# Performance work log

Hardware: AMD Instinct MI355X
Metric: run time of the kernel (lower is better)

## Reference

```python
import jax, jax.numpy as jnp
import numpy as np

N = 1_000_000
L_MAX = 8
NUM_REP = 4
N_SCALARS = 64
ROT_IN = L_MAX * 2 * 2          # 32 (num_rep_in = 2)
ROT_OUT = NUM_REP * L_MAX * 2   # 64
ROT_HID = ROT_OUT * 3           # 192
SC_HID = N_SCALARS * 3          # 192


def setup_inputs() -> dict:
    key = jax.random.key(0)
    ks = jax.random.split(key, 12)
    inp = {
        "v": jax.random.normal(ks[0], (N, 2), jnp.float32),
        "force": jax.random.normal(ks[1], (N, 2), jnp.float32),
        "is_moving": jax.random.randint(ks[2], (N,), 0, 2, jnp.int64),
        "rot_theta": jax.random.normal(ks[3], (N, L_MAX, 2, 2), jnp.float32),
        # scalar MLP params (in=4 -> 192 -> 64)
        "Ws1": jax.random.normal(ks[4], (4, SC_HID), jnp.float32) * 0.1,
        "bs1": jnp.zeros((SC_HID,), jnp.float32),
        "Ws2": jax.random.normal(ks[5], (SC_HID, N_SCALARS), jnp.float32) * 0.1,
        "bs2": jnp.zeros((N_SCALARS,), jnp.float32),
        # rot MLP params (in=32 -> 192 -> 64)
        "Wr1": jax.random.normal(ks[6], (ROT_IN, ROT_HID), jnp.float32) * 0.1,
        "br1": jnp.zeros((ROT_HID,), jnp.float32),
        "Wr2": jax.random.normal(ks[7], (ROT_HID, ROT_OUT), jnp.float32) * 0.1,
        "br2": jnp.zeros((ROT_OUT,), jnp.float32),
    }
    return inp


def _mlp(x, W1, b1, W2, b2):
    return jax.nn.relu(x @ W1 + b1) @ W2 + b2


def reference(v, force, is_moving, rot_theta, Ws1, bs1, Ws2, bs2, Wr1, br1, Wr2, br2):
    n = force.shape[0]
    force_norm = jnp.linalg.norm(force, axis=1)          # [N]
    f_hat = force / force_norm[:, None]
    v_norm = jnp.linalg.norm(v, axis=1)
    v_hat = v / v_norm[:, None]
    theta_f = jnp.arctan2(f_hat[:, 1], f_hat[:, 0])[:, None]  # [N,1]
    theta_v = jnp.arctan2(v_hat[:, 1], v_hat[:, 0])[:, None]

    one_hot = jax.nn.one_hot(is_moving, 2, dtype=force.dtype)  # [N,2]

    k = jnp.arange(1, L_MAX + 1, dtype=force.dtype)[None, :]   # [1,L]
    k_f = theta_f * k                                           # [N,L]
    k_v = theta_v * k
    # stack (cos, sin) along new axis then flatten -> [N, 2*L]
    rot_f = jnp.stack((jnp.cos(k_f), jnp.sin(k_f)), axis=2).reshape(n, L_MAX * 2)
    rot_v = jnp.stack((jnp.cos(k_v), jnp.sin(k_v)), axis=2).reshape(n, L_MAX * 2)

    scalar_features = jnp.concatenate(
        [force_norm[:, None], v_norm[:, None], one_hot], axis=1)  # [N,4]
    scalar_out = _mlp(scalar_features, Ws1, bs1, Ws2, bs2)        # [N,64]

    rot_feat = jnp.stack([rot_f, rot_v], axis=1)                  # [N,2,2L]

    # Rot_embedding2 forward
    rot_theta_inv = jnp.swapaxes(rot_theta, 2, 3)                 # [N,L,2,2]
    x = rot_feat.reshape(n, 2, L_MAX, 2)
    x = jnp.einsum('njkm,nkml->njkl', x, rot_theta_inv).reshape(n, ROT_IN)
    x = _mlp(x, Wr1, br1, Wr2, br2)                               # [N,64]
    x = x.reshape(n, NUM_REP, L_MAX, 2)
    rot_out = jnp.einsum('njkm,nkml->njkl', x, rot_theta).reshape(n, NUM_REP, L_MAX * 2)

    return scalar_out, rot_out
```

## Files before the change

kernel.cpp:

```cpp
#include <hip/hip_runtime.h>
#include <math.h>

typedef short bf16x8 __attribute__((ext_vector_type(8)));
typedef float f32x16 __attribute__((ext_vector_type(16)));
typedef float f32x4v __attribute__((ext_vector_type(4)));
typedef unsigned short u16;
typedef unsigned int u32;

__device__ __forceinline__ u16 f2bf(float x) {
    u32 u = __float_as_uint(x);
    u += 0x7FFFu + ((u >> 16) & 1u);
    return (u16)(u >> 16);
}

__device__ __forceinline__ u32 cvt_pk_bf16(float lo, float hi) {
    u32 r;
    asm("v_cvt_pk_bf16_f32 %0, %1, %2" : "=v"(r) : "v"(lo), "v"(hi));
    return r;
}

__device__ __forceinline__ void pl32_swap(u32 &x, u32 &y) {
    asm volatile("v_permlane32_swap_b32 %0, %1" : "+v"(x), "+v"(y));
}

__device__ __forceinline__ bf16x8 frag_from(u32 a, u32 b, u32 c, u32 d) {
    union { u32 u[4]; bf16x8 v; } t;
    t.u[0] = a; t.u[1] = b; t.u[2] = c; t.u[3] = d;
    return t.v;
}

__global__ void prepack_kernel(const float* __restrict__ Ws1, const float* __restrict__ bs1,
                               const float* __restrict__ Ws2, const float* __restrict__ Wr1,
                               const float* __restrict__ br1, const float* __restrict__ Wr2,
                               u16* __restrict__ ws)
{
    int idx = blockIdx.x * blockDim.x + threadIdx.x;
    if (idx >= 36864) return;
    int e = idx & 511, l = e >> 3, j = e & 7, hi = l >> 5, l31 = l & 31;
    float val = 0.0f;
    if (idx < 12288) {
        int blk = idx >> 9;
        if (blk < 18) {
            int nt = blk / 3, kstep = blk % 3;
            int h = nt * 32 + l31;
            int k = kstep * 16 + 8 * hi + j;
            if (k < 32) {
                int t = k & 3, kk = k >> 2;
                int r_old = (t >> 1) * 16 + 2 * kk + (t & 1);
                val = Wr1[r_old * 192 + h];
            } else if (k == 32) val = br1[h];
        } else {
            int h = (blk - 18) * 32 + l31;
            int k = 32 + 8 * hi + j;
            val = (k == 32) ? bs1[h] : ((k >= 33 && k <= 36) ? Ws1[(k - 33) * 192 + h] : 0.0f);
        }
    } else {
        int t = idx - 12288;
        int blk = t >> 9;
        int mlp = blk / 24, rem = blk % 24, ks = rem >> 1, nto = rem & 1;
        int k = 16 * ks + 8 * hi + j;
        int col = nto * 32 + l31;
        val = (mlp == 0 ? Wr2 : Ws2)[k * 64 + col];
    }
    ws[idx] = f2bf(val);
}

__global__ __launch_bounds__(256, 4) void node_embed_mfma(
    const float* __restrict__ v, const float* __restrict__ force,
    const int* __restrict__ is_moving, const float* __restrict__ rot_theta,
    const float* __restrict__ br2, const float* __restrict__ bs2,
    const u16* __restrict__ wpack,
    float* __restrict__ out, int n)
{
    __shared__ alignas(16)  u16   Buf[4][1280];
    __shared__ alignas(128) float Rs[4][1024];

    const int lane = threadIdx.x & 63;
    const int w    = threadIdx.x >> 6;
    const int hi   = lane >> 5;
    const int l31  = lane & 31;
    const int waveBase = blockIdx.x * 128 + w * 32;

    u16*   Xs  = &Buf[w][0];
    float* Os  = reinterpret_cast<float*>(&Buf[w][0]);
    const char* RsB = reinterpret_cast<const char*>(&Rs[w][0]);

    {
        const char* gbase = reinterpret_cast<const char*>(rot_theta);
        const u32 inner = ((u32)(lane & 7) * 16u) ^ ((u32)(lane >> 3) << 4);
        #pragma unroll
        for (int i = 0; i < 4; ++i) {
            int node_i = waveBase + i * 8 + (lane >> 3);
            node_i = min(node_i, n - 1);
            const void* src = gbase + (size_t)node_i * 128 + inner;
            __builtin_amdgcn_global_load_lds(
                (const __attribute__((address_space(1))) u32*)src,
                (__attribute__((address_space(3))) u32*)(&Rs[w][i * 256]),
                16, 0, 0);
        }
    }

    const int node = waveBase + l31;
    const int ldn  = min(node, n - 1);

    const float2 p2 = *reinterpret_cast<const float2*>((hi ? v : force) + (size_t)ldn * 2);
    const float nrm = sqrtf(p2.x * p2.x + p2.y * p2.y);
    const float c = p2.x / nrm, s = p2.y / nrm;
    const int mov = is_moving[ldn];

    asm volatile("s_waitcnt vmcnt(0)" ::: "memory");

    u16* xrow = Xs + l31 * 40;
    {
        float pc = c, ps = s;
        const u32 rowswz = (u32)(l31 & 7) << 4;
        #pragma unroll
        for (int k = 0; k < 8; ++k) {
            const u32 off = ((u32)(l31 * 128 + k * 16)) ^ rowswz;
            const float4 R = *reinterpret_cast<const float4*>(RsB + off);
            const float e0 = fmaf(R.x, pc, R.y * ps);
            const float e1 = fmaf(R.z, pc, R.w * ps);
            *reinterpret_cast<u32*>(xrow + 4 * k + 2 * hi) = cvt_pk_bf16(e0, e1);
            const float npc = pc * c - ps * s;
            ps = fmaf(ps, c, pc * s);
            pc = npc;
        }
    }
    {
        const u16 nb = f2bf(nrm);
        u32 pk1, pk2;
        if (hi == 0) { pk1 = 0x3F80u | ((u32)nb << 16);
                       pk2 = (mov == 1) ? 0x3F80u : 0u; }
        else         { pk1 = (u32)nb | ((mov == 0) ? 0x3F800000u : 0u);
                       pk2 = 0u; }
        *reinterpret_cast<u32*>(xrow + 32 + 2 * hi) = pk1;
        *reinterpret_cast<u32*>(xrow + 36 + 2 * hi) = pk2;
    }

    const bf16x8 xb0 = *reinterpret_cast<const bf16x8*>(&Xs[l31 * 40 + 8 * hi]);
    const bf16x8 xb1 = *reinterpret_cast<const bf16x8*>(&Xs[l31 * 40 + 16 + 8 * hi]);
    const bf16x8 xq4 = *reinterpret_cast<const bf16x8*>(&Xs[l31 * 40 + 32]);

    const u16* A1 = wpack;
    const u16* W2 = wpack + 12288;

    const int rowl = lane >> 4;
    const int qd   = lane & 15;

    const float b2r_a = br2[l31],      b2r_b = br2[32 + l31];
    const float b2s_a = bs2[l31],      b2s_b = bs2[32 + l31];

    #pragma unroll
    for (int mlp = 0; mlp < 2; ++mlp) {
        const float b2a = mlp ? b2s_a : b2r_a;
        const float b2b = mlp ? b2s_b : b2r_b;

        f32x16 acc0, acc1;
        #pragma unroll
        for (int r = 0; r < 16; ++r) { acc0[r] = b2a; acc1[r] = b2b; }

        #pragma unroll
        for (int a = 0; a < 6; ++a) {
            f32x16 d1;
            #pragma unroll
            for (int r = 0; r < 16; ++r) d1[r] = 0.0f;
            if (mlp == 0) {
                d1 = __builtin_amdgcn_mfma_f32_32x32x16_bf16(
                    *reinterpret_cast<const bf16x8*>(&A1[(a*3+0)*512 + lane*8]), xb0, d1, 0, 0, 0);
                d1 = __builtin_amdgcn_mfma_f32_32x32x16_bf16(
                    *reinterpret_cast<const bf16x8*>(&A1[(a*3+1)*512 + lane*8]), xb1, d1, 0, 0, 0);
                d1 = __builtin_amdgcn_mfma_f32_32x32x16_bf16(
                    *reinterpret_cast<const bf16x8*>(&A1[(a*3+2)*512 + lane*8]), xq4, d1, 0, 0, 0);
            } else {
                d1 = __builtin_amdgcn_mfma_f32_32x32x16_bf16(
                    *reinterpret_cast<const bf16x8*>(&A1[(18+a)*512 + lane*8]), xq4, d1, 0, 0, 0);
            }

            u32 q[8];
            #pragma unroll
            for (int m = 0; m < 8; ++m)
                q[m] = cvt_pk_bf16(fmaxf(d1[2*m], 0.0f), fmaxf(d1[2*m+1], 0.0f));

            #pragma unroll
            for (int b = 0; b < 2; ++b) {
                u32 p0 = q[4*b + 0], p2 = q[4*b + 2];
                u32 p1 = q[4*b + 1], p3 = q[4*b + 3];
                pl32_swap(p0, p2);
                pl32_swap(p1, p3);
                const bf16x8 af = frag_from(p0, p1, p2, p3);
                const int ks = 2*a + b;
                acc0 = __builtin_amdgcn_mfma_f32_32x32x16_bf16(
                    af, *reinterpret_cast<const bf16x8*>(&W2[(mlp*24 + ks*2 + 0)*512 + lane*8]),
                    acc0, 0, 0, 0);
                acc1 = __builtin_amdgcn_mfma_f32_32x32x16_bf16(
                    af, *reinterpret_cast<const bf16x8*>(&W2[(mlp*24 + ks*2 + 1)*512 + lane*8]),
                    acc1, 0, 0, 0);
            }
        }

        #pragma unroll
        for (int rq = 0; rq < 4; ++rq) {
            #pragma unroll
            for (int rr = 0; rr < 4; ++rr) {
                const int r = rq * 4 + rr;
                Os[(rr + 4*hi) * 72 + l31]      = acc0[r];
                Os[(rr + 4*hi) * 72 + 32 + l31] = acc1[r];
            }
            #pragma unroll
            for (int g = 0; g < 2; ++g) {
                const int row   = g * 4 + rowl;
                const int srow  = rq * 8 + row;
                const int node0 = waveBase + srow;
                float4 o = *reinterpret_cast<const float4*>(&Os[row * 72 + 4 * qd]);
                if (mlp == 0) {
                    const u32 roff = ((u32)(srow * 128 + (qd & 3) * 32))
                                   ^ ((u32)(srow & 7) << 4);
                    const float4 Ra = *reinterpret_cast<const float4*>(RsB + roff);
                    const float4 Rc = *reinterpret_cast<const float4*>(RsB + (roff ^ 16u));
                    {
                        const float a0 = o.x, b0 = o.y;
                        o.x = fmaf(a0, Ra.x, b0 * Ra.z); o.y = fmaf(a0, Ra.y, b0 * Ra.w);
                    }
                    {
                        const float a0 = o.z, b0 = o.w;
                        o.z = fmaf(a0, Rc.x, b0 * Rc.z); o.w = fmaf(a0, Rc.y, b0 * Rc.w);
                    }
                }
                if (node0 < n) {
                    float* dst = out + (mlp ? (size_t)0 : (size_t)n * 64)
                                     + (size_t)node0 * 64 + 4 * qd;
                    f32x4v ov;
                    ov[0] = o.x; ov[1] = o.y; ov[2] = o.z; ov[3] = o.w;
                    __builtin_nontemporal_store(ov, reinterpret_cast<f32x4v*>(dst));
                }
            }
        }
    }
}

__global__ __launch_bounds__(256) void node_embed_valu(
    const float* __restrict__ v, const float* __restrict__ force,
    const int* __restrict__ is_moving, const float* __restrict__ rot_theta,
    const float* __restrict__ Ws1, const float* __restrict__ bs1,
    const float* __restrict__ Ws2, const float* __restrict__ bs2,
    const float* __restrict__ Wr1, const float* __restrict__ br1,
    const float* __restrict__ Wr2, const float* __restrict__ br2,
    float* __restrict__ out, int n)
{
    const int node = blockIdx.x * blockDim.x + threadIdx.x;
    if (node >= n) return;
    const float2 f2 = *reinterpret_cast<const float2*>(force + (size_t)node * 2);
    const float2 v2 = *reinterpret_cast<const float2*>(v     + (size_t)node * 2);
    const float fn = sqrtf(f2.x * f2.x + f2.y * f2.y);
    const float vn = sqrtf(v2.x * v2.x + v2.y * v2.y);
    const float cf = f2.x / fn, sf = f2.y / fn;
    const float cv = v2.x / vn, sv = v2.y / vn;
    const int mov = is_moving[node];
    float rotf[16], rotv[16];
    rotf[0] = cf; rotf[1] = sf; rotv[0] = cv; rotv[1] = sv;
    #pragma unroll
    for (int k = 1; k < 8; ++k) {
        rotf[2*k]   = rotf[2*k-2] * cf - rotf[2*k-1] * sf;
        rotf[2*k+1] = rotf[2*k-1] * cf + rotf[2*k-2] * sf;
        rotv[2*k]   = rotv[2*k-2] * cv - rotv[2*k-1] * sv;
        rotv[2*k+1] = rotv[2*k-1] * cv + rotv[2*k-2] * sv;
    }
    const float* Rb = rot_theta + (size_t)node * 32;
    float x_in[32];
    #pragma unroll
    for (int k = 0; k < 8; ++k) {
        const float4 R = *reinterpret_cast<const float4*>(Rb + k * 4);
        { const float a = rotf[2*k], b = rotf[2*k+1];
          x_in[2*k] = fmaf(R.x,a,R.y*b); x_in[2*k+1] = fmaf(R.z,a,R.w*b); }
        { const float a = rotv[2*k], b = rotv[2*k+1];
          x_in[16+2*k] = fmaf(R.x,a,R.y*b); x_in[16+2*k+1] = fmaf(R.z,a,R.w*b); }
    }
    float acc[64];
    #pragma unroll
    for (int j = 0; j < 64; ++j) acc[j] = br2[j];
    for (int h = 0; h < 192; h += 4) {
        float hid[4];
        #pragma unroll
        for (int u = 0; u < 4; ++u) {
            float t = br1[h+u];
            #pragma unroll
            for (int i = 0; i < 32; ++i) t = fmaf(x_in[i], Wr1[i*192+h+u], t);
            hid[u] = fmaxf(t, 0.0f);
        }
        #pragma unroll
        for (int j = 0; j < 64; ++j) {
            float t = acc[j];
            #pragma unroll
            for (int u = 0; u < 4; ++u) t = fmaf(hid[u], Wr2[(h+u)*64+j], t);
            acc[j] = t;
        }
    }
    #pragma unroll
    for (int k = 0; k < 8; ++k) {
        const float4 R = *reinterpret_cast<const float4*>(Rb + k * 4);
        #pragma unroll
        for (int j = 0; j < 4; ++j) {
            const int p = j*16 + 2*k;
            const float a = acc[p], b = acc[p+1];
            acc[p] = fmaf(a,R.x,b*R.z); acc[p+1] = fmaf(a,R.y,b*R.w);
        }
    }
    float* orow = out + (size_t)n * 64 + (size_t)node * 64;
    #pragma unroll
    for (int j = 0; j < 16; ++j)
        *reinterpret_cast<float4*>(orow + 4*j) =
            make_float4(acc[4*j], acc[4*j+1], acc[4*j+2], acc[4*j+3]);
    const float s0 = fn, s1 = vn, s2 = (mov==0)?1.f:0.f, s3 = (mov==1)?1.f:0.f;
    #pragma unroll
    for (int j = 0; j < 64; ++j) acc[j] = bs2[j];
    for (int h = 0; h < 192; h += 4) {
        float hid[4];
        #pragma unroll
        for (int u = 0; u < 4; ++u) {
            float t = bs1[h+u];
            t = fmaf(s0, Ws1[0*192+h+u], t); t = fmaf(s1, Ws1[1*192+h+u], t);
            t = fmaf(s2, Ws1[2*192+h+u], t); t = fmaf(s3, Ws1[3*192+h+u], t);
            hid[u] = fmaxf(t, 0.0f);
        }
        #pragma unroll
        for (int j = 0; j < 64; ++j) {
            float t = acc[j];
            #pragma unroll
            for (int u = 0; u < 4; ++u) t = fmaf(hid[u], Ws2[(h+u)*64+j], t);
            acc[j] = t;
        }
    }
    orow = out + (size_t)node * 64;
    #pragma unroll
    for (int j = 0; j < 16; ++j)
        *reinterpret_cast<float4*>(orow + 4*j) =
            make_float4(acc[4*j], acc[4*j+1], acc[4*j+2], acc[4*j+3]);
}

extern "C" void kernel_launch(void* const* d_in, const int* in_sizes, int n_in,
                              void* d_out, int out_size, void* d_ws, size_t ws_size,
                              hipStream_t stream) {
    const int n = in_sizes[0] / 2;
    if (ws_size >= 36864 * sizeof(u16)) {
        hipLaunchKernelGGL(prepack_kernel, dim3(144), dim3(256), 0, stream,
                           (const float*)d_in[4],
                           (const float*)d_in[5],
                           (const float*)d_in[6],
                           (const float*)d_in[8],
                           (const float*)d_in[9],
                           (const float*)d_in[10],
                           (u16*)d_ws);
        hipLaunchKernelGGL(node_embed_mfma, dim3((n + 127) / 128), dim3(256), 0, stream,
                           (const float*)d_in[0], (const float*)d_in[1],
                           (const int*)d_in[2],   (const float*)d_in[3],
                           (const float*)d_in[11],
                           (const float*)d_in[7],
                           (const u16*)d_ws, (float*)d_out, n);
    } else {
        hipLaunchKernelGGL(node_embed_valu, dim3((n + 255) / 256), dim3(256), 0, stream,
                           (const float*)d_in[0], (const float*)d_in[1],
                           (const int*)d_in[2],   (const float*)d_in[3],
                           (const float*)d_in[4], (const float*)d_in[5],
                           (const float*)d_in[6], (const float*)d_in[7],
                           (const float*)d_in[8], (const float*)d_in[9],
                           (const float*)d_in[10],(const float*)d_in[11],
                           (float*)d_out, n);
    }
}
```

Before: 146.7 us.

## Process two 32-node subtiles per wave with upfront loads of both tiles

Each wave now handles 64 nodes as two 32-node subtiles. The rot_theta LDS loads and the per-node force, v and is_moving loads for both subtiles are issued together before a single wait, halving the grid size. The aim is more memory-level parallelism per wave and less per-block fixed overhead. In exchange LDS use per block doubles, occupancy drops from 4 to 3 blocks per CU, and the second subtile's loads are not overlapped with the first subtile's compute because of the single vmcnt(0) wait.

```diff
diff --git a/kernel.cpp b/kernel.cpp
--- a/kernel.cpp
+++ b/kernel.cpp
@@ -65,7 +65,7 @@
     ws[idx] = f2bf(val);
 }
 
-__global__ __launch_bounds__(256, 4) void node_embed_mfma(
+__global__ __launch_bounds__(256, 3) void node_embed_mfma(
     const float* __restrict__ v, const float* __restrict__ force,
     const int* __restrict__ is_moving, const float* __restrict__ rot_theta,
     const float* __restrict__ br2, const float* __restrict__ bs2,
@@ -73,73 +73,41 @@
     float* __restrict__ out, int n)
 {
     __shared__ alignas(16)  u16   Buf[4][1280];
-    __shared__ alignas(128) float Rs[4][1024];
+    __shared__ alignas(128) float Rs[4][2048];
 
     const int lane = threadIdx.x & 63;
     const int w    = threadIdx.x >> 6;
     const int hi   = lane >> 5;
     const int l31  = lane & 31;
-    const int waveBase = blockIdx.x * 128 + w * 32;
+    const int base0 = blockIdx.x * 256 + w * 64;
+    const int base1 = base0 + 32;
 
     u16*   Xs  = &Buf[w][0];
     float* Os  = reinterpret_cast<float*>(&Buf[w][0]);
-    const char* RsB = reinterpret_cast<const char*>(&Rs[w][0]);
-
-    {
-        const char* gbase = reinterpret_cast<const char*>(rot_theta);
-        const u32 inner = ((u32)(lane & 7) * 16u) ^ ((u32)(lane >> 3) << 4);
+
+    const u32 inner = ((u32)(lane & 7) * 16u) ^ ((u32)(lane >> 3) << 4);
+    const char* gbase = reinterpret_cast<const char*>(rot_theta);
+
+    auto issue_rs = [&](int tbase, int buf) {
         #pragma unroll
         for (int i = 0; i < 4; ++i) {
-            int node_i = waveBase + i * 8 + (lane >> 3);
-            node_i = min(node_i, n - 1);
+            int node_i = min(tbase + i * 8 + (lane >> 3), n - 1);
             const void* src = gbase + (size_t)node_i * 128 + inner;
             __builtin_amdgcn_global_load_lds(
                 (const __attribute__((address_space(1))) u32*)src,
-                (__attribute__((address_space(3))) u32*)(&Rs[w][i * 256]),
+                (__attribute__((address_space(3))) u32*)(&Rs[w][buf * 1024 + i * 256]),
                 16, 0, 0);
         }
-    }
-
-    const int node = waveBase + l31;
-    const int ldn  = min(node, n - 1);
-
-    const float2 p2 = *reinterpret_cast<const float2*>((hi ? v : force) + (size_t)ldn * 2);
-    const float nrm = sqrtf(p2.x * p2.x + p2.y * p2.y);
-    const float c = p2.x / nrm, s = p2.y / nrm;
-    const int mov = is_moving[ldn];
-
-    asm volatile("s_waitcnt vmcnt(0)" ::: "memory");
-
-    u16* xrow = Xs + l31 * 40;
-    {
-        float pc = c, ps = s;
-        const u32 rowswz = (u32)(l31 & 7) << 4;
-        #pragma unroll
-        for (int k = 0; k < 8; ++k) {
-            const u32 off = ((u32)(l31 * 128 + k * 16)) ^ rowswz;
-            const float4 R = *reinterpret_cast<const float4*>(RsB + off);
-            const float e0 = fmaf(R.x, pc, R.y * ps);
-            const float e1 = fmaf(R.z, pc, R.w * ps);
-            *reinterpret_cast<u32*>(xrow + 4 * k + 2 * hi) = cvt_pk_bf16(e0, e1);
-            const float npc = pc * c - ps * s;
-            ps = fmaf(ps, c, pc * s);
-            pc = npc;
-        }
-    }
-    {
-        const u16 nb = f2bf(nrm);
-        u32 pk1, pk2;
-        if (hi == 0) { pk1 = 0x3F80u | ((u32)nb << 16);
-                       pk2 = (mov == 1) ? 0x3F80u : 0u; }
-        else         { pk1 = (u32)nb | ((mov == 0) ? 0x3F800000u : 0u);
-                       pk2 = 0u; }
-        *reinterpret_cast<u32*>(xrow + 32 + 2 * hi) = pk1;
-        *reinterpret_cast<u32*>(xrow + 36 + 2 * hi) = pk2;
-    }
-
-    const bf16x8 xb0 = *reinterpret_cast<const bf16x8*>(&Xs[l31 * 40 + 8 * hi]);
-    const bf16x8 xb1 = *reinterpret_cast<const bf16x8*>(&Xs[l31 * 40 + 16 + 8 * hi]);
-    const bf16x8 xq4 = *reinterpret_cast<const bf16x8*>(&Xs[l31 * 40 + 32]);
+    };
+
+    issue_rs(base0, 0);
+    issue_rs(base1, 1);
+    const int ldnA = min(base0 + l31, n - 1);
+    const int ldnB = min(base1 + l31, n - 1);
+    const float2 p2A = *reinterpret_cast<const float2*>((hi ? v : force) + (size_t)ldnA * 2);
+    const float2 p2B = *reinterpret_cast<const float2*>((hi ? v : force) + (size_t)ldnB * 2);
+    const int movA = is_moving[ldnA];
+    const int movB = is_moving[ldnB];
 
     const u16* A1 = wpack;
     const u16* W2 = wpack + 12288;
@@ -147,95 +115,136 @@
     const int rowl = lane >> 4;
     const int qd   = lane & 15;
 
-    const float b2r_a = br2[l31],      b2r_b = br2[32 + l31];
-    const float b2s_a = bs2[l31],      b2s_b = bs2[32 + l31];
-
-    #pragma unroll
-    for (int mlp = 0; mlp < 2; ++mlp) {
-        const float b2a = mlp ? b2s_a : b2r_a;
-        const float b2b = mlp ? b2s_b : b2r_b;
-
-        f32x16 acc0, acc1;
-        #pragma unroll
-        for (int r = 0; r < 16; ++r) { acc0[r] = b2a; acc1[r] = b2b; }
-
-        #pragma unroll
-        for (int a = 0; a < 6; ++a) {
-            f32x16 d1;
-            #pragma unroll
-            for (int r = 0; r < 16; ++r) d1[r] = 0.0f;
-            if (mlp == 0) {
-                d1 = __builtin_amdgcn_mfma_f32_32x32x16_bf16(
-                    *reinterpret_cast<const bf16x8*>(&A1[(a*3+0)*512 + lane*8]), xb0, d1, 0, 0, 0);
-                d1 = __builtin_amdgcn_mfma_f32_32x32x16_bf16(
-                    *reinterpret_cast<const bf16x8*>(&A1[(a*3+1)*512 + lane*8]), xb1, d1, 0, 0, 0);
-                d1 = __builtin_amdgcn_mfma_f32_32x32x16_bf16(
-                    *reinterpret_cast<const bf16x8*>(&A1[(a*3+2)*512 + lane*8]), xq4, d1, 0, 0, 0);
-            } else {
-                d1 = __builtin_amdgcn_mfma_f32_32x32x16_bf16(
-                    *reinterpret_cast<const bf16x8*>(&A1[(18+a)*512 + lane*8]), xq4, d1, 0, 0, 0);
+    const float b2r_a = br2[l31], b2r_b = br2[32 + l31];
+    const float b2s_a = bs2[l31], b2s_b = bs2[32 + l31];
+
+    asm volatile("s_waitcnt vmcnt(0)" ::: "memory");
+
+    auto subtile = [&](int waveBase, float2 p2, int mov, const char* RsB) {
+        const float nrm = sqrtf(p2.x * p2.x + p2.y * p2.y);
+        const float c = p2.x / nrm, s = p2.y / nrm;
+
+        u16* xrow = Xs + l31 * 40;
+        {
+            float pc = c, ps = s;
+            const u32 rowswz = (u32)(l31 & 7) << 4;
+            #pragma unroll
+            for (int k = 0; k < 8; ++k) {
+                const u32 off = ((u32)(l31 * 128 + k * 16)) ^ rowswz;
+                const float4 R = *reinterpret_cast<const float4*>(RsB + off);
+                const float e0 = fmaf(R.x, pc, R.y * ps);
+                const float e1 = fmaf(R.z, pc, R.w * ps);
+                *reinterpret_cast<u32*>(xrow + 4 * k + 2 * hi) = cvt_pk_bf16(e0, e1);
+                const float npc = pc * c - ps * s;
+                ps = fmaf(ps, c, pc * s);
+                pc = npc;
             }
-
-            u32 q[8];
-            #pragma unroll
-            for (int m = 0; m < 8; ++m)
-                q[m] = cvt_pk_bf16(fmaxf(d1[2*m], 0.0f), fmaxf(d1[2*m+1], 0.0f));
-
-            #pragma unroll
-            for (int b = 0; b < 2; ++b) {
-                u32 p0 = q[4*b + 0], p2 = q[4*b + 2];
-                u32 p1 = q[4*b + 1], p3 = q[4*b + 3];
-                pl32_swap(p0, p2);
-                pl32_swap(p1, p3);
-                const bf16x8 af = frag_from(p0, p1, p2, p3);
-                const int ks = 2*a + b;
-                acc0 = __builtin_amdgcn_mfma_f32_32x32x16_bf16(
-                    af, *reinterpret_cast<const bf16x8*>(&W2[(mlp*24 + ks*2 + 0)*512 + lane*8]),
-                    acc0, 0, 0, 0);
-                acc1 = __builtin_amdgcn_mfma_f32_32x32x16_bf16(
-                    af, *reinterpret_cast<const bf16x8*>(&W2[(mlp*24 + ks*2 + 1)*512 + lane*8]),
-                    acc1, 0, 0, 0);
+        }
+        {
+            const u16 nb = f2bf(nrm);
+            u32 pk1, pk2;
+            if (hi == 0) { pk1 = 0x3F80u | ((u32)nb << 16);
+                           pk2 = (mov == 1) ? 0x3F80u : 0u; }
+            else         { pk1 = (u32)nb | ((mov == 0) ? 0x3F800000u : 0u);
+                           pk2 = 0u; }
+            *reinterpret_cast<u32*>(xrow + 32 + 2 * hi) = pk1;
+            *reinterpret_cast<u32*>(xrow + 36 + 2 * hi) = pk2;
+        }
+
+        const bf16x8 xb0 = *reinterpret_cast<const bf16x8*>(&Xs[l31 * 40 + 8 * hi]);
+        const bf16x8 xb1 = *reinterpret_cast<const bf16x8*>(&Xs[l31 * 40 + 16 + 8 * hi]);
+        const bf16x8 xq4 = *reinterpret_cast<const bf16x8*>(&Xs[l31 * 40 + 32]);
+
+        #pragma unroll
+        for (int mlp = 0; mlp < 2; ++mlp) {
+            const float b2a = mlp ? b2s_a : b2r_a;
+            const float b2b = mlp ? b2s_b : b2r_b;
+
+            f32x16 acc0, acc1;
+            #pragma unroll
+            for (int r = 0; r < 16; ++r) { acc0[r] = b2a; acc1[r] = b2b; }
+
+            #pragma unroll
+            for (int a = 0; a < 6; ++a) {
+                f32x16 d1;
+                #pragma unroll
+                for (int r = 0; r < 16; ++r) d1[r] = 0.0f;
+                if (mlp == 0) {
+                    d1 = __builtin_amdgcn_mfma_f32_32x32x16_bf16(
+                        *reinterpret_cast<const bf16x8*>(&A1[(a*3+0)*512 + lane*8]), xb0, d1, 0, 0, 0);
+                    d1 = __builtin_amdgcn_mfma_f32_32x32x16_bf16(
+                        *reinterpret_cast<const bf16x8*>(&A1[(a*3+1)*512 + lane*8]), xb1, d1, 0, 0, 0);
+                    d1 = __builtin_amdgcn_mfma_f32_32x32x16_bf16(
+                        *reinterpret_cast<const bf16x8*>(&A1[(a*3+2)*512 + lane*8]), xq4, d1, 0, 0, 0);
+                } else {
+                    d1 = __builtin_amdgcn_mfma_f32_32x32x16_bf16(
+                        *reinterpret_cast<const bf16x8*>(&A1[(18+a)*512 + lane*8]), xq4, d1, 0, 0, 0);
+                }
+
+                u32 q[8];
+                #pragma unroll
+                for (int m = 0; m < 8; ++m)
+                    q[m] = cvt_pk_bf16(fmaxf(d1[2*m], 0.0f), fmaxf(d1[2*m+1], 0.0f));
+
+                #pragma unroll
+                for (int b = 0; b < 2; ++b) {
+                    u32 p0 = q[4*b + 0], p2_ = q[4*b + 2];
+                    u32 p1 = q[4*b + 1], p3 = q[4*b + 3];
+                    pl32_swap(p0, p2_);
+                    pl32_swap(p1, p3);
+                    const bf16x8 af = frag_from(p0, p1, p2_, p3);
+                    const int ks = 2*a + b;
+                    acc0 = __builtin_amdgcn_mfma_f32_32x32x16_bf16(
+                        af, *reinterpret_cast<const bf16x8*>(&W2[(mlp*24 + ks*2 + 0)*512 + lane*8]),
+                        acc0, 0, 0, 0);
+                    acc1 = __builtin_amdgcn_mfma_f32_32x32x16_bf16(
+                        af, *reinterpret_cast<const bf16x8*>(&W2[(mlp*24 + ks*2 + 1)*512 + lane*8]),
+                        acc1, 0, 0, 0);
+                }
             }
-        }
-
-        #pragma unroll
-        for (int rq = 0; rq < 4; ++rq) {
-            #pragma unroll
-            for (int rr = 0; rr < 4; ++rr) {
-                const int r = rq * 4 + rr;
-                Os[(rr + 4*hi) * 72 + l31]      = acc0[r];
-                Os[(rr + 4*hi) * 72 + 32 + l31] = acc1[r];
-            }
-            #pragma unroll
-            for (int g = 0; g < 2; ++g) {
-                const int row   = g * 4 + rowl;
-                const int srow  = rq * 8 + row;
-                const int node0 = waveBase + srow;
-                float4 o = *reinterpret_cast<const float4*>(&Os[row * 72 + 4 * qd]);
-                if (mlp == 0) {
-                    const u32 roff = ((u32)(srow * 128 + (qd & 3) * 32))
-                                   ^ ((u32)(srow & 7) << 4);
-                    const float4 Ra = *reinterpret_cast<const float4*>(RsB + roff);
-                    const float4 Rc = *reinterpret_cast<const float4*>(RsB + (roff ^ 16u));
-                    {
-                        const float a0 = o.x, b0 = o.y;
-                        o.x = fmaf(a0, Ra.x, b0 * Ra.z); o.y = fmaf(a0, Ra.y, b0 * Ra.w);
+
+            #pragma unroll
+            for (int rq = 0; rq < 4; ++rq) {
+                #pragma unroll
+                for (int rr = 0; rr < 4; ++rr) {
+                    const int r = rq * 4 + rr;
+                    Os[(rr + 4*hi) * 72 + l31]      = acc0[r];
+                    Os[(rr + 4*hi) * 72 + 32 + l31] = acc1[r];
+                }
+                #pragma unroll
+                for (int g = 0; g < 2; ++g) {
+                    const int row   = g * 4 + rowl;
+                    const int srow  = rq * 8 + row;
+                    const int node0 = waveBase + srow;
+                    float4 o = *reinterpret_cast<const float4*>(&Os[row * 72 + 4 * qd]);
+                    if (mlp == 0) {
+                        const u32 roff = ((u32)(srow * 128 + (qd & 3) * 32))
+                                       ^ ((u32)(srow & 7) << 4);
+                        const float4 Ra = *reinterpret_cast<const float4*>(RsB + roff);
+                        const float4 Rc = *reinterpret_cast<const float4*>(RsB + (roff ^ 16u));
+                        {
+                            const float a0 = o.x, b0 = o.y;
+                            o.x = fmaf(a0, Ra.x, b0 * Ra.z); o.y = fmaf(a0, Ra.y, b0 * Ra.w);
+                        }
+                        {
+                            const float a0 = o.z, b0 = o.w;
+                            o.z = fmaf(a0, Rc.x, b0 * Rc.z); o.w = fmaf(a0, Rc.y, b0 * Rc.w);
+                        }
                     }
-                    {
-                        const float a0 = o.z, b0 = o.w;
-                        o.z = fmaf(a0, Rc.x, b0 * Rc.z); o.w = fmaf(a0, Rc.y, b0 * Rc.w);
+                    if (node0 < n) {
+                        float* dst = out + (mlp ? (size_t)0 : (size_t)n * 64)
+                                         + (size_t)node0 * 64 + 4 * qd;
+                        f32x4v ov;
+                        ov[0] = o.x; ov[1] = o.y; ov[2] = o.z; ov[3] = o.w;
+                        __builtin_nontemporal_store(ov, reinterpret_cast<f32x4v*>(dst));
                     }
                 }
-                if (node0 < n) {
-                    float* dst = out + (mlp ? (size_t)0 : (size_t)n * 64)
-                                     + (size_t)node0 * 64 + 4 * qd;
-                    f32x4v ov;
-                    ov[0] = o.x; ov[1] = o.y; ov[2] = o.z; ov[3] = o.w;
-                    __builtin_nontemporal_store(ov, reinterpret_cast<f32x4v*>(dst));
-                }
             }
         }
-    }
+    };
+
+    subtile(base0, p2A, movA, reinterpret_cast<const char*>(&Rs[w][0]));
+    subtile(base1, p2B, movB, reinterpret_cast<const char*>(&Rs[w][1024]));
 }
 
 __global__ __launch_bounds__(256) void node_embed_valu(
@@ -350,7 +359,7 @@
                            (const float*)d_in[9],
                            (const float*)d_in[10],
                            (u16*)d_ws);
-        hipLaunchKernelGGL(node_embed_mfma, dim3((n + 127) / 128), dim3(256), 0, stream,
+        hipLaunchKernelGGL(node_embed_mfma, dim3((n + 255) / 256), dim3(256), 0, stream,
                            (const float*)d_in[0], (const float*)d_in[1],
                            (const int*)d_in[2],   (const float*)d_in[3],
                            (const float*)d_in[11],
```

Result: slower. 203.0 us (+38.4%).
